# Optimization experiments

Hardware: AMD Instinct MI355X
Metric: run time of the kernel (lower is better)

## Reference

```python
import math
import jax, jax.numpy as jnp
import numpy as np

B, T, DIM = 2, 2048, 2048
HEADS, HEAD_DIM = 16, 128
KV_GROUPS = 4
N_KV = HEADS // KV_GROUPS  # 4
LATENT = 512
SEL_TOPK, SEL_HEADS, SEL_DIM = 64, 1, 64
SOFTCAP = 30.0
EPS = 1e-6


def _alibi_slopes(n):
    def pot(p):
        start = 2.0 ** (-(2.0 ** (-(math.log2(p) - 3))))
        return [start * start ** i for i in range(p)]
    if math.log2(n).is_integer():
        return pot(n)
    cp = 2 ** int(math.floor(math.log2(n)))
    s = pot(cp)
    s += _alibi_slopes(2 * cp)[0::2][: n - cp]
    return s


def _alibi_bias(h, t):
    slopes = jnp.asarray(_alibi_slopes(h), jnp.float32)
    pos = jnp.arange(t)
    dist = jnp.clip(pos[:, None] - pos[None, :], 0, None).astype(jnp.float32)  # causal clamp_min(0)
    return -slopes[:, None, None] * dist  # (H,T,T)


def _rope_emb(t, d):
    inv = 1.0 / (10000.0 ** (jnp.arange(0, d, 2, dtype=jnp.float32) / d))
    f = jnp.arange(t, dtype=jnp.float32)[:, None] * inv[None, :]
    return jnp.concatenate([f, f], axis=-1)  # (T, D)


def _apply_rotary(x, emb):
    # x: (B,T,H,D); replicates RotaryPositionalEncoding.apply_rotary exactly
    cos = jnp.cos(emb)[None, :, None, :]
    sin = jnp.sin(emb)[None, :, None, :]
    x1, x2 = x[..., 0::2], x[..., 1::2]
    c, s = cos[..., 0::2], sin[..., 0::2]
    r = jnp.stack([x1 * c - x2 * s, x1 * s + x2 * c], axis=-1)
    return r.reshape(x.shape)


def _rmsnorm(x, w):
    return x * jax.lax.rsqrt(jnp.mean(x * x, axis=-1, keepdims=True) + EPS) * w


def _forward(x, w_q, b_q, w_down, b_down, w_up, b_up, w_o, b_o, qn_w, kn_w, gate_w, gate_b):
    b, t, _ = x.shape
    # MLA projections
    q = (x @ w_q + b_q).reshape(b, t, HEADS, HEAD_DIM)
    kv = (x @ w_down + b_down) @ w_up + b_up  # (B,T,2*N_KV*D)
    k = kv[..., : N_KV * HEAD_DIM].reshape(b, t, N_KV, HEAD_DIM)
    v = kv[..., N_KV * HEAD_DIM:].reshape(b, t, N_KV, HEAD_DIM)
    # QK RMS-norm + RoPE
    q = _rmsnorm(q, qn_w)
    k = _rmsnorm(k, kn_w)
    emb = _rope_emb(t, HEAD_DIM)
    q = _apply_rotary(q, emb)
    k = _apply_rotary(k, emb)
    # GQA expand kv heads
    k = jnp.repeat(k, KV_GROUPS, axis=2)
    v = jnp.repeat(v, KV_GROUPS, axis=2)
    q = q.transpose(0, 2, 1, 3)  # (B,H,T,D)
    k = k.transpose(0, 2, 1, 3)
    v = v.transpose(0, 2, 1, 3)
    # selector top-k mask (detached)
    qs = jax.lax.stop_gradient(q[:, :SEL_HEADS, :, :SEL_DIM].astype(jnp.float32))
    ks = jax.lax.stop_gradient(k[:, :SEL_HEADS, :, :SEL_DIM].astype(jnp.float32))
    s = jnp.einsum('bhqd,bhkd->bhqk', qs, ks) / math.sqrt(SEL_DIM)
    tri = jnp.triu(jnp.ones((t, t), bool), 1)  # future positions
    s = jnp.where(tri, -jnp.inf, s)
    idx = jax.lax.top_k(s, SEL_TOPK)[1]  # (B,hs,T,K)
    sel = jnp.zeros((b, SEL_HEADS, t, t), bool)
    bi = jnp.arange(b)[:, None, None, None]
    hi = jnp.arange(SEL_HEADS)[None, :, None, None]
    ti = jnp.arange(t)[None, None, :, None]
    sel = sel.at[bi, hi, ti, idx].set(True)
    sel = sel | jnp.eye(t, dtype=bool)[None, None]  # always keep diagonal
    sel = sel & ~tri  # causal
    sel = jnp.any(sel, axis=1, keepdims=True)  # broadcast over heads (h_sel < h)
    amask = jnp.where(sel, 0.0, -jnp.inf).astype(jnp.float32)
    # attention with softcap + ALiBi
    scores = jnp.einsum('bhqd,bhkd->bhqk', q, k) / math.sqrt(HEAD_DIM)
    scores = jnp.tanh(scores / SOFTCAP) * SOFTCAP
    scores = scores + _alibi_bias(HEADS, t)[None] + amask
    attn = jax.nn.softmax(scores, axis=-1)
    y = jnp.einsum('bhqk,bhkd->bhqd', attn, v)
    # per-head dense sigmoid gating on output
    gate = jax.nn.sigmoid(jnp.einsum('bhtd,hde->bhte', y, gate_w) + gate_b[None, :, None, :])
    y = (y * gate).transpose(0, 2, 1, 3).reshape(b, t, HEADS * HEAD_DIM)
    return y @ w_o + b_o


def setup_inputs() -> dict:
    key = jax.random.key(0)
    ks = jax.random.split(key, 6)
    sd = 0.02
    return {
        'x': jax.random.normal(ks[0], (B, T, DIM), jnp.float32),
        'w_q': jax.random.normal(ks[1], (DIM, HEADS * HEAD_DIM), jnp.float32) * sd,
        'b_q': jnp.zeros((HEADS * HEAD_DIM,), jnp.float32),
        'w_down': jax.random.normal(ks[2], (DIM, LATENT), jnp.float32) * sd,
        'b_down': jnp.zeros((LATENT,), jnp.float32),
        'w_up': jax.random.normal(ks[3], (LATENT, 2 * N_KV * HEAD_DIM), jnp.float32) * sd,
        'b_up': jnp.zeros((2 * N_KV * HEAD_DIM,), jnp.float32),
        'w_o': jax.random.normal(ks[4], (HEADS * HEAD_DIM, DIM), jnp.float32) * sd,
        'b_o': jnp.zeros((DIM,), jnp.float32),
        'qn_w': jnp.ones((HEAD_DIM,), jnp.float32),
        'kn_w': jnp.ones((HEAD_DIM,), jnp.float32),
        'gate_w': jax.random.normal(ks[5], (HEADS, HEAD_DIM, HEAD_DIM), jnp.float32) * (1.0 / math.sqrt(HEAD_DIM)),
        'gate_b': jnp.zeros((HEADS, HEAD_DIM), jnp.float32),
    }


def reference(x, w_q, b_q, w_down, b_down, w_up, b_up, w_o, b_o, qn_w, kn_w, gate_w, gate_b):
    return _forward(x, w_q, b_q, w_down, b_down, w_up, b_up, w_o, b_o, qn_w, kn_w, gate_w, gate_b)
```

## Files before the change

kernel.cpp:

```cpp
#include <hip/hip_runtime.h>
#include <math.h>

#define T_SEQ 2048
#define BATCH 2
#define NHEADS 16
#define HD 128
#define NKV 4

typedef __bf16 bf16x8 __attribute__((ext_vector_type(8)));
typedef float f32x4 __attribute__((ext_vector_type(4)));

__device__ inline unsigned short bf16rne(float f) {
  unsigned u = __float_as_uint(f);
  unsigned r = (u + 0x7FFFu + ((u >> 16) & 1u)) >> 16;
  return (unsigned short)r;
}

__device__ inline float bflo(unsigned u) {
  return __uint_as_float(u << 16);
}
__device__ inline float bfhi(unsigned u) {
  return __uint_as_float(u & 0xFFFF0000u);
}

__device__ inline void gload_lds16(const void* g, void* l) {
  __builtin_amdgcn_global_load_lds(
      (__attribute__((address_space(1))) void*)const_cast<void*>(g),
      (__attribute__((address_space(3))) void*)l, 16, 0, 0);
}

#define ENC_NEGINF 0x007FFFFFu
__device__ inline unsigned enc32(float v) {
  unsigned u = __float_as_uint(v);
  return (u & 0x80000000u) ? ~u : (u | 0x80000000u);
}

__global__ void rope_table_kernel(float* __restrict__ tab) {
  int t = blockIdx.x;
  int i = threadIdx.x;
  int j = (2 * i) & 63;
  float y = (float)pow(10000.0, (double)j / 64.0);
  float invf = 1.0f / y;
  float angle = (float)t * invf;
  double a = (double)angle;
  tab[(t * 64 + i) * 2 + 0] = (float)cos(a);
  tab[(t * 64 + i) * 2 + 1] = (float)sin(a);
}

__global__ __launch_bounds__(128) void norm_rope_kernel(
    float* __restrict__ base, const float* __restrict__ w,
    const float* __restrict__ tab, int Hloc, int rowStride) {
  int blk = blockIdx.x;
  int h = blk % Hloc;
  int bt = blk / Hloc;
  int t = bt & (T_SEQ - 1);
  float* row = base + (size_t)bt * rowStride + h * HD;
  int d = threadIdx.x;
  float v = row[d];
  __shared__ float red[128];
  red[d] = v * v;
  __syncthreads();
#pragma unroll
  for (int off = 64; off > 0; off >>= 1) {
    if (d < off) red[d] += red[d + off];
    __syncthreads();
  }
  float ssum = red[0];
  __syncthreads();
  float inv = 1.0f / sqrtf(ssum / 128.0f + 1e-6f);
  float xn = v * inv * w[d];
  red[d] = xn;
  __syncthreads();
  int p = d >> 1;
  float c  = tab[(t * 64 + p) * 2 + 0];
  float sn = tab[(t * 64 + p) * 2 + 1];
  float x1 = red[p * 2], x2 = red[p * 2 + 1];
  row[d] = ((d & 1) == 0) ? (x1 * c - x2 * sn) : (x1 * sn + x2 * c);
}

__global__ __launch_bounds__(128) void kvnorm_rope_kernel(
    float* __restrict__ base, const float* __restrict__ w,
    const float* __restrict__ tab, unsigned short* __restrict__ kvb) {
  int blk = blockIdx.x;
  int h = blk % 4;
  int bt = blk / 4;
  int t = bt & (T_SEQ - 1);
  float* row = base + (size_t)bt * 1024 + h * HD;
  int d = threadIdx.x;
  float v = row[d];
  __shared__ float red[128];
  red[d] = v * v;
  __syncthreads();
#pragma unroll
  for (int off = 64; off > 0; off >>= 1) {
    if (d < off) red[d] += red[d + off];
    __syncthreads();
  }
  float ssum = red[0];
  __syncthreads();
  float inv = 1.0f / sqrtf(ssum / 128.0f + 1e-6f);
  float xn = v * inv * w[d];
  red[d] = xn;
  __syncthreads();
  int p = d >> 1;
  float c  = tab[(t * 64 + p) * 2 + 0];
  float sn = tab[(t * 64 + p) * 2 + 1];
  float x1 = red[p * 2], x2 = red[p * 2 + 1];
  float out = ((d & 1) == 0) ? (x1 * c - x2 * sn) : (x1 * sn + x2 * c);
  row[d] = out;
  size_t kb = (size_t)bt * 1024 + h * HD + d;
  kvb[kb] = bf16rne(out);
  float vv = base[(size_t)bt * 1024 + 512 + h * HD + d];
  kvb[(size_t)bt * 1024 + 512 + h * HD + d] = bf16rne(vv);
}

__global__ __launch_bounds__(256) void qnorm_rope_kernel(
    float* __restrict__ base, const float* __restrict__ w,
    const float* __restrict__ tab) {
  int row = blockIdx.x * 4 + (threadIdx.x >> 6);
  int lane = threadIdx.x & 63;
  int h = row & 15;
  int bt = row >> 4;
  int t = bt & (T_SEQ - 1);
  float* rp = base + (size_t)bt * 2048 + h * HD;
  float2 v = *(const float2*)(rp + 2 * lane);
  float ss = v.x * v.x + v.y * v.y;
#pragma unroll
  for (int off = 32; off > 0; off >>= 1) ss += __shfl_xor(ss, off);
  float inv = 1.0f / sqrtf(ss / 128.0f + 1e-6f);
  float2 wv = *(const float2*)(w + 2 * lane);
  float x1 = v.x * inv * wv.x;
  float x2 = v.y * inv * wv.y;
  float2 cs = *(const float2*)(tab + (t * 64 + lane) * 2);
  float2 o;
  o.x = x1 * cs.x - x2 * cs.y;
  o.y = x1 * cs.y + x2 * cs.x;
  *(float2*)(rp + 2 * lane) = o;
}

#define BKG 16
__global__ __launch_bounds__(256) void sgemm3_kernel(
    const float* __restrict__ A,
    const float* __restrict__ W1, const float* __restrict__ bias1,
    float* __restrict__ C1, int ldw1, int ldc1, int nx1,
    const float* __restrict__ W2, const float* __restrict__ bias2,
    float* __restrict__ C2, int ldw2, int ldc2, int K) {
  __shared__ float As[BKG][68];
  __shared__ float Bs[BKG][68];
  int bx = blockIdx.x;
  const float* W; const float* bias; float* C; int ldw, ldc, n0;
  if (bx < nx1) {
    W = W1; bias = bias1; C = C1; ldw = ldw1; ldc = ldc1; n0 = bx * 64;
  } else {
    W = W2; bias = bias2; C = C2; ldw = ldw2; ldc = ldc2;
    n0 = (bx - nx1) * 64;
  }
  int tid = threadIdx.x;
  int tx = tid & 15;
  int ty = tid >> 4;
  int m0 = blockIdx.y * 64;
  int ar = tid >> 2, ac = (tid & 3) * 4;
  int brr = tid >> 4, bc = (tid & 15) * 4;
  const float* Ap = A + (size_t)(m0 + ar) * K + ac;
  const float* Wp = W + (size_t)brr * ldw + n0 + bc;
  float acc[4][4] = {};
  float4 av = *(const float4*)(Ap);
  float4 wv = *(const float4*)(Wp);
  for (int k0 = 0; k0 < K; k0 += BKG) {
    As[ac + 0][ar] = av.x; As[ac + 1][ar] = av.y;
    As[ac + 2][ar] = av.z; As[ac + 3][ar] = av.w;
    *(float4*)&Bs[brr][bc] = wv;
    __syncthreads();
    if (k0 + BKG < K) {
      av = *(const float4*)(Ap + k0 + BKG);
      wv = *(const float4*)(Wp + (size_t)(k0 + BKG) * ldw);
    }
#pragma unroll
    for (int kk = 0; kk < BKG; kk++) {
      float4 a = *(const float4*)&As[kk][ty * 4];
      float4 b = *(const float4*)&Bs[kk][tx * 4];
      float aa[4] = {a.x, a.y, a.z, a.w};
      float bb[4] = {b.x, b.y, b.z, b.w};
#pragma unroll
      for (int i = 0; i < 4; i++)
#pragma unroll
        for (int j = 0; j < 4; j++) acc[i][j] += aa[i] * bb[j];
    }
    __syncthreads();
  }
  float4 bv = *(const float4*)&bias[n0 + tx * 4];
  float bb[4] = {bv.x, bv.y, bv.z, bv.w};
#pragma unroll
  for (int i = 0; i < 4; i++) {
    float4 o;
    o.x = acc[i][0] + bb[0];
    o.y = acc[i][1] + bb[1];
    o.z = acc[i][2] + bb[2];
    o.w = acc[i][3] + bb[3];
    *(float4*)&C[(size_t)(m0 + ty * 4 + i) * ldc + n0 + tx * 4] = o;
  }
}

__global__ __launch_bounds__(256) void mfma_gemm_bt(
    const unsigned short* __restrict__ A,
    const unsigned short* __restrict__ BT,
    const float* __restrict__ bias,
    float* __restrict__ C,
    int M, int N, int K) {
  __shared__ bf16x8 lA[16][64];
  __shared__ bf16x8 lB[16][64];
  int tid = threadIdx.x;
  int w = tid >> 6, lane = tid & 63;
  int nb = gridDim.x * gridDim.y;
  int bid = blockIdx.y * gridDim.x + blockIdx.x;
  int cpx = nb >> 3;
  int sw = (bid & 7) * cpx + (bid >> 3);
  int bxs = sw % gridDim.x;
  int bys = sw / gridDim.x;
  int m0 = bys * 128, n0 = bxs * 128;
  int wm = w >> 1, wn = w & 1;
  f32x4 acc[4][4] = {};
  int sr = lane & 15;
  int sk = (lane >> 4) * 8;
  const unsigned short* Abase = A + (size_t)(m0 + sr) * K + sk;
  const unsigned short* Bbase = BT + (size_t)(n0 + sr) * K + sk;

  for (int k0 = 0; k0 < K; k0 += 64) {
    __syncthreads();
#pragma unroll
    for (int c = 0; c < 4; c++) {
      int ch = w * 4 + c;
      int tt = ch >> 1, kk = ch & 1;
      gload_lds16(Abase + (size_t)(tt * 16) * K + k0 + kk * 32, &lA[ch][0]);
      gload_lds16(Bbase + (size_t)(tt * 16) * K + k0 + kk * 32, &lB[ch][0]);
    }
    __syncthreads();
#pragma unroll
    for (int kk = 0; kk < 2; kk++) {
      bf16x8 af[4], bfr[4];
#pragma unroll
      for (int t = 0; t < 4; t++) {
        af[t]  = lA[(wm * 4 + t) * 2 + kk][lane];
        bfr[t] = lB[(wn * 4 + t) * 2 + kk][lane];
      }
#pragma unroll
      for (int i = 0; i < 4; i++)
#pragma unroll
        for (int j = 0; j < 4; j++)
          acc[i][j] = __builtin_amdgcn_mfma_f32_16x16x32_bf16(
              af[i], bfr[j], acc[i][j], 0, 0, 0);
    }
  }
  int col0 = n0 + wn * 64 + (lane & 15);
  int row0 = m0 + wm * 64 + (lane >> 4) * 4;
#pragma unroll
  for (int j = 0; j < 4; j++) {
    float bv = bias[col0 + j * 16];
#pragma unroll
    for (int i = 0; i < 4; i++) {
#pragma unroll
      for (int r = 0; r < 4; r++)
        C[(size_t)(row0 + i * 16 + r) * N + col0 + j * 16] = acc[i][j][r] + bv;
    }
  }
}

__global__ __launch_bounds__(256) void convert_bf16_kernel(
    const float* __restrict__ X, unsigned short* __restrict__ Y, int n4) {
  int i = blockIdx.x * 256 + threadIdx.x;
  if (i >= n4) return;
  float4 v = ((const float4*)X)[i];
  ushort4 o;
  o.x = bf16rne(v.x); o.y = bf16rne(v.y);
  o.z = bf16rne(v.z); o.w = bf16rne(v.w);
  ((ushort4*)Y)[i] = o;
}

__global__ __launch_bounds__(256) void transpose_bf16_kernel(
    const float* __restrict__ W, unsigned short* __restrict__ WT,
    int K, int N) {
  __shared__ unsigned short t[32][33];
  int k0 = blockIdx.y * 32, n0 = blockIdx.x * 32;
  int tid = threadIdx.x;
#pragma unroll
  for (int i = 0; i < 4; i++) {
    int idx = tid + i * 256;
    int r = idx >> 5, c = idx & 31;
    t[c][r] = bf16rne(W[(size_t)(k0 + r) * N + n0 + c]);
  }
  __syncthreads();
#pragma unroll
  for (int i = 0; i < 4; i++) {
    int idx = tid + i * 256;
    int r = idx >> 5, c = idx & 31;
    WT[(size_t)(n0 + r) * K + k0 + c] = t[r][c];
  }
}

__global__ __launch_bounds__(256) void score_kernel(
    const float* __restrict__ qsel,
    const float* __restrict__ kv,
    unsigned* __restrict__ S) {
  int tc = blockIdx.x, tr = blockIdx.y;
  int b = blockIdx.z;
  if (tc > tr || tr == 0) return;
  unsigned* Sb = S + (size_t)b * T_SEQ * T_SEQ;
  __shared__ float qsT[64][68];
  __shared__ float ksT[64][68];
  int tid = threadIdx.x;
  int r0 = tr * 64, c0 = tc * 64;
#pragma unroll
  for (int u = 0; u < 16; u++) {
    int idx = u * 256 + tid;
    int row = idx >> 6, d = idx & 63;
    qsT[d][row] = qsel[((size_t)(b * T_SEQ + r0 + row)) * 128 + d];
  }
#pragma unroll
  for (int u = 0; u < 16; u++) {
    int idx = u * 256 + tid;
    int c = idx >> 6, d = idx & 63;
    ksT[d][c] = kv[((size_t)(b * T_SEQ + c0 + c)) * 1024 + d];
  }
  __syncthreads();
  int tx = tid & 15, ty = tid >> 4;
  float acc[4][4] = {};
  for (int d = 0; d < 64; d++) {
    float4 qv = *(const float4*)&qsT[d][ty * 4];
    float4 kx = *(const float4*)&ksT[d][tx * 4];
    float qq[4] = {qv.x, qv.y, qv.z, qv.w};
    float kk[4] = {kx.x, kx.y, kx.z, kx.w};
#pragma unroll
    for (int i = 0; i < 4; i++)
#pragma unroll
      for (int j = 0; j < 4; j++) acc[i][j] += qq[i] * kk[j];
  }
#pragma unroll
  for (int i = 0; i < 4; i++) {
    int r = r0 + ty * 4 + i;
    uint4 o;
    int c = c0 + tx * 4;
    o.x = (c + 0 <= r) ? enc32(acc[i][0] * 0.125f) : ENC_NEGINF;
    o.y = (c + 1 <= r) ? enc32(acc[i][1] * 0.125f) : ENC_NEGINF;
    o.z = (c + 2 <= r) ? enc32(acc[i][2] * 0.125f) : ENC_NEGINF;
    o.w = (c + 3 <= r) ? enc32(acc[i][3] * 0.125f) : ENC_NEGINF;
    *(uint4*)&Sb[(size_t)r * 2048 + c] = o;
  }
}

__global__ __launch_bounds__(256) void select_topk_kernel(
    const unsigned* __restrict__ S,
    int* __restrict__ sel_cnt, int* __restrict__ sel_idx) {
  int b = blockIdx.x >> 9;
  int blk = blockIdx.x & 511;
  const unsigned* Sb = S + (size_t)b * T_SEQ * T_SEQ;
  int r0 = blk * 4;
  int tid = threadIdx.x;

  if (r0 < 64) {
    for (int j = 0; j < 4; j++) {
      int r = r0 + j;
      int row = b * T_SEQ + r;
      if (tid == 0) sel_cnt[row] = r + 1;
      for (int c = tid; c <= r; c += 256) sel_idx[row * 66 + c] = c;
    }
    return;
  }

  int wv = tid >> 6, lane = tid & 63;
  int rr = r0 + wv;
  int row = b * T_SEQ + rr;
  int imax = rr >> 6;

  unsigned e[32];
  const unsigned* Sp = Sb + (size_t)rr * 2048 + lane;
#pragma unroll
  for (int i = 0; i < 32; i++) e[i] = (i <= imax) ? Sp[i * 64] : ENC_NEGINF;

  unsigned t = 0;
  for (int bit = 31; bit >= 0; --bit) {
    unsigned cand = t | (1u << bit);
    int cnt = 0;
#pragma unroll
    for (int i = 0; i < 32; i++) cnt += (e[i] >= cand) ? 1 : 0;
#pragma unroll
    for (int off = 1; off < 64; off <<= 1) cnt += __shfl_xor(cnt, off);
    if (cnt >= 64) t = cand;
  }

  unsigned long long below = (lane == 63) ? 0x7FFFFFFFFFFFFFFFull
                                          : ((1ull << lane) - 1ull);
  bool hasdiag = false;
  int base = 0;
#pragma unroll
  for (int i = 0; i < 32; i++) {
    int c = i * 64 + lane;
    bool wn = (e[i] > t);
    unsigned long long m = __ballot(wn);
    if (wn) {
      int slot = base + (int)__popcll(m & below);
      sel_idx[(size_t)row * 66 + slot] = c;
      if (c == rr) hasdiag = true;
    }
    base += (int)__popcll(m);
  }
  int g = base;
  int need = 64 - g;
  int tb = 0;
#pragma unroll
  for (int i = 0; i < 32; i++) {
    int c = i * 64 + lane;
    bool tie = (e[i] == t);
    unsigned long long m = __ballot(tie);
    int rank = tb + (int)__popcll(m & below);
    if (tie && rank < need) {
      sel_idx[(size_t)row * 66 + g + rank] = c;
      if (c == rr) hasdiag = true;
    }
    tb += (int)__popcll(m);
  }
  unsigned long long hd = __ballot(hasdiag);
  if (lane == 0) {
    sel_cnt[row] = hd ? 64 : 65;
    if (!hd) sel_idx[(size_t)row * 66 + 64] = rr;
  }
}

__global__ __launch_bounds__(256) void attn_kernel(
    const float* __restrict__ q,
    const unsigned short* __restrict__ kvb,
    const int* __restrict__ sel_cnt, const int* __restrict__ sel_idx,
    float* __restrict__ yg) {
  int blk = blockIdx.x;
  int g = blk & 3;
  int br = blk >> 2;
  int b = br >> 11;
  int r = br & (T_SEQ - 1);
  int tid = threadIdx.x;
  int lane = tid & 63, wv = tid >> 6;
  int H = g * 4 + wv;

  __shared__ unsigned kls[65 * 64];
  __shared__ float pbuf[4][68];
  __shared__ int idxs[66];

  int cnt = sel_cnt[br];
  if (tid < 66) idxs[tid] = (tid < cnt) ? sel_idx[(size_t)br * 66 + tid] : 0;
  __syncthreads();

  for (int c = tid; c < 65 * 16; c += 256) {
    int row = c >> 4, part = c & 15;
    uint4 kd = make_uint4(0u, 0u, 0u, 0u);
    if (row < cnt) {
      const unsigned short* gp = kvb
          + ((size_t)(b * T_SEQ + idxs[row])) * 1024 + g * HD + part * 8;
      kd = *(const uint4*)gp;
    }
    int slot = part ^ (row & 15);
    *(uint4*)&kls[row * 64 + slot * 4] = kd;
  }
  __syncthreads();

  double sd = 1.0;
  for (int i = 0; i <= H; i++) sd *= 0.70710678118654752440;
  float slope = (float)sd;

  const float* qrow = q + (size_t)br * 2048 + H * HD;

  int kidx = idxs[min(lane, cnt - 1)];
  int swz = lane & 15;
  const unsigned* kr = &kls[lane * 64];
  float acc = 0.f;
#pragma unroll
  for (int dd = 0; dd < 16; dd++) {
    uint4 kb = *(const uint4*)&kr[(dd ^ swz) * 4];
    float4 qa = *(const float4*)(qrow + dd * 8);
    float4 qb = *(const float4*)(qrow + dd * 8 + 4);
    acc += qa.x * bflo(kb.x) + qa.y * bfhi(kb.x);
    acc += qa.z * bflo(kb.y) + qa.w * bfhi(kb.y);
    acc += qb.x * bflo(kb.z) + qb.y * bfhi(kb.z);
    acc += qb.z * bflo(kb.w) + qb.w * bfhi(kb.w);
  }
  float sca = acc / sqrtf(128.0f);
  float tch = tanhf(sca / 30.0f) * 30.0f;
  float s = (lane < cnt) ? (tch - slope * (float)(r - kidx)) : -INFINITY;

  float stail = -INFINITY;
  if (cnt == 65) {
    int i64 = idxs[64];
    unsigned u = kls[64 * 64 + lane];
    float2 qt = *(const float2*)(qrow + 2 * lane);
    float ta = qt.x * bflo(u) + qt.y * bfhi(u);
#pragma unroll
    for (int off = 32; off > 0; off >>= 1) ta += __shfl_xor(ta, off);
    stail = tanhf(ta / sqrtf(128.0f) / 30.0f) * 30.0f
            - slope * (float)(r - i64);
  }

  float m = s;
#pragma unroll
  for (int off = 32; off > 0; off >>= 1) m = fmaxf(m, __shfl_xor(m, off));
  m = fmaxf(m, stail);
  float e = (lane < cnt) ? expf(s - m) : 0.f;
  float sum = e;
#pragma unroll
  for (int off = 32; off > 0; off >>= 1) sum += __shfl_xor(sum, off);
  float et = (cnt == 65) ? expf(stail - m) : 0.f;
  sum += et;
  pbuf[wv][lane] = e / sum;
  if (lane == 0) pbuf[wv][64] = et / sum;
  if (lane >= 1 && lane <= 3) pbuf[wv][64 + lane] = 0.f;

  const unsigned short* vbase = kvb + (size_t)b * T_SEQ * 1024 + 512 + g * HD;
  float y0 = 0.f, y1 = 0.f;
  int jmax = (cnt + 3) >> 2;
  for (int j4 = 0; j4 < jmax; j4++) {
    float4 p4 = *(const float4*)&pbuf[wv][j4 * 4];
    float pp[4] = {p4.x, p4.y, p4.z, p4.w};
#pragma unroll
    for (int t = 0; t < 4; t++) {
      int ij = idxs[min(j4 * 4 + t, cnt - 1)];
      unsigned u = *(const unsigned*)(vbase + (size_t)ij * 1024 + 2 * lane);
      y0 += pp[t] * bflo(u);
      y1 += pp[t] * bfhi(u);
    }
  }
  float2 o;
  o.x = y0;
  o.y = y1;
  *(float2*)(yg + (size_t)br * 2048 + H * HD + 2 * lane) = o;
}

__global__ __launch_bounds__(256) void gate_kernel(
    const float* __restrict__ yg, unsigned short* __restrict__ ygb,
    const float* __restrict__ gw, const float* __restrict__ gb) {
  int blk = blockIdx.x;
  int h = blk & 15;
  int bt0 = (blk >> 4) * 32;
  int tid = threadIdx.x;
  __shared__ float ys[32][128];
  for (int i = tid; i < 32 * 128; i += 256) {
    int rr = i >> 7, d = i & 127;
    ys[rr][d] = yg[(size_t)(bt0 + rr) * 2048 + h * HD + d];
  }
  __syncthreads();
  int e = tid & 127;
  int rblk = tid >> 7;
  const float* gwp = gw + (size_t)h * 16384 + e;
  float acc[16] = {};
  for (int d = 0; d < 128; d += 4) {
    float w0 = gwp[(size_t)(d + 0) * 128];
    float w1 = gwp[(size_t)(d + 1) * 128];
    float w2 = gwp[(size_t)(d + 2) * 128];
    float w3 = gwp[(size_t)(d + 3) * 128];
#pragma unroll
    for (int k = 0; k < 16; k++) {
      float4 y4 = *(const float4*)&ys[rblk * 16 + k][d];
      acc[k] += y4.x * w0;
      acc[k] += y4.y * w1;
      acc[k] += y4.z * w2;
      acc[k] += y4.w * w3;
    }
  }
  float bb = gb[h * 128 + e];
#pragma unroll
  for (int k = 0; k < 16; k++) {
    int rr = rblk * 16 + k;
    float gate = 1.f / (1.f + expf(-(acc[k] + bb)));
    ygb[(size_t)(bt0 + rr) * 2048 + h * HD + e] = bf16rne(ys[rr][e] * gate);
  }
}

extern "C" void kernel_launch(void* const* d_in, const int* in_sizes, int n_in,
                              void* d_out, int out_size, void* d_ws, size_t ws_size,
                              hipStream_t stream) {
  const float* x      = (const float*)d_in[0];
  const float* w_q    = (const float*)d_in[1];
  const float* b_q    = (const float*)d_in[2];
  const float* w_down = (const float*)d_in[3];
  const float* b_down = (const float*)d_in[4];
  const float* w_up   = (const float*)d_in[5];
  const float* b_up   = (const float*)d_in[6];
  const float* w_o    = (const float*)d_in[7];
  const float* b_o    = (const float*)d_in[8];
  const float* qn_w   = (const float*)d_in[9];
  const float* kn_w   = (const float*)d_in[10];
  const float* gate_w = (const float*)d_in[11];
  const float* gate_b = (const float*)d_in[12];

  float* ws    = (float*)d_ws;
  float* kvbuf = ws;
  float* yg    = ws + 4194304;
  float* dlat  = yg;
  unsigned* Sfull = (unsigned*)yg;
  float* tab   = ws + 12582912;
  int*   cnt   = (int*)(ws + 12845056);
  int*   sidx  = cnt + 4096;
  float* qsel  = ws + 13120000;
  unsigned short* xb  = (unsigned short*)(ws + 13906432);
  unsigned short* dlatb = xb;
  unsigned short* ygb = xb;
  unsigned short* wT  = xb + 8388608;
  unsigned short* wupT = wT;
  unsigned short* kvb  = wT;

  float* qbuf = (float*)d_out;
  const int BT = BATCH * T_SEQ;

  rope_table_kernel<<<T_SEQ, 64, 0, stream>>>(tab);
  convert_bf16_kernel<<<8192, 256, 0, stream>>>(x, xb, 2097152);
  transpose_bf16_kernel<<<dim3(64, 64), 256, 0, stream>>>(w_q, wT, 2048, 2048);
  mfma_gemm_bt<<<dim3(16, 32), 256, 0, stream>>>(xb, wT, b_q, qbuf,
                                                 BT, 2048, 2048);
  sgemm3_kernel<<<dim3(10, 64), 256, 0, stream>>>(
      x, w_q, b_q, qsel, 2048, 128, 2,
      w_down, b_down, dlat, 512, 512, 2048);
  convert_bf16_kernel<<<2048, 256, 0, stream>>>(dlat, dlatb, 524288);
  transpose_bf16_kernel<<<dim3(32, 16), 256, 0, stream>>>(w_up, wupT,
                                                          512, 1024);
  mfma_gemm_bt<<<dim3(8, 32), 256, 0, stream>>>(dlatb, wupT, b_up, kvbuf,
                                                BT, 1024, 512);
  sgemm3_kernel<<<dim3(2, 64), 256, 0, stream>>>(
      dlat, w_up, b_up, kvbuf, 1024, 1024, 2,
      w_up, b_up, kvbuf, 1024, 1024, 512);
  qnorm_rope_kernel<<<BT * 4, 256, 0, stream>>>(qbuf, qn_w, tab);
  norm_rope_kernel<<<BT, 128, 0, stream>>>(qsel, qn_w, tab, 1, 128);
  kvnorm_rope_kernel<<<BT * 4, 128, 0, stream>>>(kvbuf, kn_w, tab, kvb);
  score_kernel<<<dim3(32, 32, 2), 256, 0, stream>>>(qsel, kvbuf, Sfull);
  select_topk_kernel<<<1024, 256, 0, stream>>>(Sfull, cnt, sidx);
  attn_kernel<<<BT * 4, 256, 0, stream>>>(qbuf, kvb, cnt, sidx, yg);
  gate_kernel<<<(BT / 32) * 16, 256, 0, stream>>>(yg, ygb, gate_w, gate_b);
  transpose_bf16_kernel<<<dim3(64, 64), 256, 0, stream>>>(w_o, wT, 2048, 2048);
  mfma_gemm_bt<<<dim3(16, 32), 256, 0, stream>>>(ygb, wT, b_o, (float*)d_out,
                                                 BT, 2048, 2048);
}
```

Measured before the change: 725.9 us.

## Merge independent fp32 and bf16 MFMA GEMMs into combined heterogeneous launches

Replaces the separate MFMA q-projection GEMM and fp32 sgemm (selector/down projection) with one launch whose blocks dispatch to either body by block index, and likewise for the up-projection. The fp32 and bf16 GEMMs then run concurrently on the GPU, filling idle CUs and removing launch gaps. In the second fused kernel the MFMA path skips the first 128 columns, which the fp32 path computes, so that column block is no longer written twice. Shared memory is unified at 32KB per block, which may reduce occupancy for the sgemm blocks.

```diff
diff --git a/kernel.cpp b/kernel.cpp
--- a/kernel.cpp
+++ b/kernel.cpp
@@ -139,26 +139,15 @@
 }
 
 #define BKG 16
-__global__ __launch_bounds__(256) void sgemm3_kernel(
-    const float* __restrict__ A,
-    const float* __restrict__ W1, const float* __restrict__ bias1,
-    float* __restrict__ C1, int ldw1, int ldc1, int nx1,
-    const float* __restrict__ W2, const float* __restrict__ bias2,
-    float* __restrict__ C2, int ldw2, int ldc2, int K) {
-  __shared__ float As[BKG][68];
-  __shared__ float Bs[BKG][68];
-  int bx = blockIdx.x;
-  const float* W; const float* bias; float* C; int ldw, ldc, n0;
-  if (bx < nx1) {
-    W = W1; bias = bias1; C = C1; ldw = ldw1; ldc = ldc1; n0 = bx * 64;
-  } else {
-    W = W2; bias = bias2; C = C2; ldw = ldw2; ldc = ldc2;
-    n0 = (bx - nx1) * 64;
-  }
+__device__ __forceinline__ void sgemm_body(
+    const float* __restrict__ A, const float* __restrict__ W,
+    const float* __restrict__ bias, float* __restrict__ C,
+    int ldw, int ldc, int n0, int m0, int K, char* smem) {
+  float (*As)[68] = (float (*)[68])smem;
+  float (*Bs)[68] = (float (*)[68])(smem + 4352);
   int tid = threadIdx.x;
   int tx = tid & 15;
   int ty = tid >> 4;
-  int m0 = blockIdx.y * 64;
   int ar = tid >> 2, ac = (tid & 3) * 4;
   int brr = tid >> 4, bc = (tid & 15) * 4;
   const float* Ap = A + (size_t)(m0 + ar) * K + ac;
@@ -201,67 +190,120 @@
   }
 }
 
-__global__ __launch_bounds__(256) void mfma_gemm_bt(
+__device__ __forceinline__ void mfma_body(
     const unsigned short* __restrict__ A,
     const unsigned short* __restrict__ BT,
     const float* __restrict__ bias,
     float* __restrict__ C,
-    int M, int N, int K) {
-  __shared__ bf16x8 lA[16][64];
-  __shared__ bf16x8 lB[16][64];
+    int N, int K, int m0, int n0, char* smem) {
+  bf16x8 (*lA)[64] = (bf16x8 (*)[64])smem;
+  bf16x8 (*lB)[64] = (bf16x8 (*)[64])(smem + 16384);
   int tid = threadIdx.x;
   int w = tid >> 6, lane = tid & 63;
+  int wm = w >> 1, wn = w & 1;
+  f32x4 acc[4][4] = {};
+  int sr = lane & 15;
+  int sk = (lane >> 4) * 8;
+  const unsigned short* Abase = A + (size_t)(m0 + sr) * K + sk;
+  const unsigned short* Bbase = BT + (size_t)(n0 + sr) * K + sk;
+
+  for (int k0 = 0; k0 < K; k0 += 64) {
+    __syncthreads();
+#pragma unroll
+    for (int c = 0; c < 4; c++) {
+      int ch = w * 4 + c;
+      int tt = ch >> 1, kk = ch & 1;
+      gload_lds16(Abase + (size_t)(tt * 16) * K + k0 + kk * 32, &lA[ch][0]);
+      gload_lds16(Bbase + (size_t)(tt * 16) * K + k0 + kk * 32, &lB[ch][0]);
+    }
+    __syncthreads();
+#pragma unroll
+    for (int kk = 0; kk < 2; kk++) {
+      bf16x8 af[4], bfr[4];
+#pragma unroll
+      for (int t = 0; t < 4; t++) {
+        af[t]  = lA[(wm * 4 + t) * 2 + kk][lane];
+        bfr[t] = lB[(wn * 4 + t) * 2 + kk][lane];
+      }
+#pragma unroll
+      for (int i = 0; i < 4; i++)
+#pragma unroll
+        for (int j = 0; j < 4; j++)
+          acc[i][j] = __builtin_amdgcn_mfma_f32_16x16x32_bf16(
+              af[i], bfr[j], acc[i][j], 0, 0, 0);
+    }
+  }
+  int col0 = n0 + wn * 64 + (lane & 15);
+  int row0 = m0 + wm * 64 + (lane >> 4) * 4;
+#pragma unroll
+  for (int j = 0; j < 4; j++) {
+    float bv = bias[col0 + j * 16];
+#pragma unroll
+    for (int i = 0; i < 4; i++) {
+#pragma unroll
+      for (int r = 0; r < 4; r++)
+        C[(size_t)(row0 + i * 16 + r) * N + col0 + j * 16] = acc[i][j][r] + bv;
+    }
+  }
+}
+
+__global__ __launch_bounds__(256) void mfma_gemm_bt(
+    const unsigned short* __restrict__ A,
+    const unsigned short* __restrict__ BT,
+    const float* __restrict__ bias, float* __restrict__ C,
+    int M, int N, int K) {
+  __shared__ __align__(16) char smem[32768];
   int nb = gridDim.x * gridDim.y;
   int bid = blockIdx.y * gridDim.x + blockIdx.x;
   int cpx = nb >> 3;
   int sw = (bid & 7) * cpx + (bid >> 3);
   int bxs = sw % gridDim.x;
   int bys = sw / gridDim.x;
-  int m0 = bys * 128, n0 = bxs * 128;
-  int wm = w >> 1, wn = w & 1;
-  f32x4 acc[4][4] = {};
-  int sr = lane & 15;
-  int sk = (lane >> 4) * 8;
-  const unsigned short* Abase = A + (size_t)(m0 + sr) * K + sk;
-  const unsigned short* Bbase = BT + (size_t)(n0 + sr) * K + sk;
-
-  for (int k0 = 0; k0 < K; k0 += 64) {
-    __syncthreads();
-#pragma unroll
-    for (int c = 0; c < 4; c++) {
-      int ch = w * 4 + c;
-      int tt = ch >> 1, kk = ch & 1;
-      gload_lds16(Abase + (size_t)(tt * 16) * K + k0 + kk * 32, &lA[ch][0]);
-      gload_lds16(Bbase + (size_t)(tt * 16) * K + k0 + kk * 32, &lB[ch][0]);
-    }
-    __syncthreads();
-#pragma unroll
-    for (int kk = 0; kk < 2; kk++) {
-      bf16x8 af[4], bfr[4];
-#pragma unroll
-      for (int t = 0; t < 4; t++) {
-        af[t]  = lA[(wm * 4 + t) * 2 + kk][lane];
-        bfr[t] = lB[(wn * 4 + t) * 2 + kk][lane];
-      }
-#pragma unroll
-      for (int i = 0; i < 4; i++)
-#pragma unroll
-        for (int j = 0; j < 4; j++)
-          acc[i][j] = __builtin_amdgcn_mfma_f32_16x16x32_bf16(
-              af[i], bfr[j], acc[i][j], 0, 0, 0);
-    }
-  }
-  int col0 = n0 + wn * 64 + (lane & 15);
-  int row0 = m0 + wm * 64 + (lane >> 4) * 4;
-#pragma unroll
-  for (int j = 0; j < 4; j++) {
-    float bv = bias[col0 + j * 16];
-#pragma unroll
-    for (int i = 0; i < 4; i++) {
-#pragma unroll
-      for (int r = 0; r < 4; r++)
-        C[(size_t)(row0 + i * 16 + r) * N + col0 + j * 16] = acc[i][j][r] + bv;
-    }
+  mfma_body(A, BT, bias, C, N, K, bys * 128, bxs * 128, smem);
+}
+
+__global__ __launch_bounds__(256) void fat1_kernel(
+    const float* __restrict__ x,
+    const float* __restrict__ w_q, const float* __restrict__ b_q,
+    float* __restrict__ qsel,
+    const float* __restrict__ w_down, const float* __restrict__ b_down,
+    float* __restrict__ dlat,
+    const unsigned short* __restrict__ xb,
+    const unsigned short* __restrict__ wT,
+    float* __restrict__ qbuf) {
+  __shared__ __align__(16) char smem[32768];
+  int bid = blockIdx.x;
+  if (bid < 640) {
+    int bx = bid % 10, by = bid / 10;
+    if (bx < 2)
+      sgemm_body(x, w_q, b_q, qsel, 2048, 128, bx * 64, by * 64, 2048, smem);
+    else
+      sgemm_body(x, w_down, b_down, dlat, 512, 512, (bx - 2) * 64, by * 64,
+                 2048, smem);
+  } else {
+    int mb = bid - 640;
+    int bx = mb & 15, by = mb >> 4;
+    mfma_body(xb, wT, b_q, qbuf, 2048, 2048, by * 128, bx * 128, smem);
+  }
+}
+
+__global__ __launch_bounds__(256) void fat2_kernel(
+    const float* __restrict__ dlat,
+    const float* __restrict__ w_up, const float* __restrict__ b_up,
+    float* __restrict__ kvbuf,
+    const unsigned short* __restrict__ dlatb,
+    const unsigned short* __restrict__ wupT) {
+  __shared__ __align__(16) char smem[32768];
+  int bid = blockIdx.x;
+  if (bid < 128) {
+    int bx = bid & 1, by = bid >> 1;
+    sgemm_body(dlat, w_up, b_up, kvbuf, 1024, 1024, bx * 64, by * 64, 512,
+               smem);
+  } else {
+    int mb = bid - 128;
+    int bx = mb % 7, by = mb / 7;
+    mfma_body(dlatb, wupT, b_up, kvbuf, 1024, 512, by * 128, (bx + 1) * 128,
+              smem);
   }
 }
 
@@ -609,19 +651,13 @@
   rope_table_kernel<<<T_SEQ, 64, 0, stream>>>(tab);
   convert_bf16_kernel<<<8192, 256, 0, stream>>>(x, xb, 2097152);
   transpose_bf16_kernel<<<dim3(64, 64), 256, 0, stream>>>(w_q, wT, 2048, 2048);
-  mfma_gemm_bt<<<dim3(16, 32), 256, 0, stream>>>(xb, wT, b_q, qbuf,
-                                                 BT, 2048, 2048);
-  sgemm3_kernel<<<dim3(10, 64), 256, 0, stream>>>(
-      x, w_q, b_q, qsel, 2048, 128, 2,
-      w_down, b_down, dlat, 512, 512, 2048);
+  fat1_kernel<<<1152, 256, 0, stream>>>(x, w_q, b_q, qsel,
+                                        w_down, b_down, dlat,
+                                        xb, wT, qbuf);
   convert_bf16_kernel<<<2048, 256, 0, stream>>>(dlat, dlatb, 524288);
   transpose_bf16_kernel<<<dim3(32, 16), 256, 0, stream>>>(w_up, wupT,
                                                           512, 1024);
-  mfma_gemm_bt<<<dim3(8, 32), 256, 0, stream>>>(dlatb, wupT, b_up, kvbuf,
-                                                BT, 1024, 512);
-  sgemm3_kernel<<<dim3(2, 64), 256, 0, stream>>>(
-      dlat, w_up, b_up, kvbuf, 1024, 1024, 2,
-      w_up, b_up, kvbuf, 1024, 1024, 512);
+  fat2_kernel<<<352, 256, 0, stream>>>(dlat, w_up, b_up, kvbuf, dlatb, wupT);
   qnorm_rope_kernel<<<BT * 4, 256, 0, stream>>>(qbuf, qn_w, tab);
   norm_rope_kernel<<<BT, 128, 0, stream>>>(qsel, qn_w, tab, 1, 128);
   kvnorm_rope_kernel<<<BT * 4, 128, 0, stream>>>(kvbuf, kn_w, tab, kvb);
```

New measurement: 715.8 us. About the same (-1.4%).
